# Kernel optimization log

Hardware: AMD Instinct MI355X
Metric: run time of the kernel (lower is better)

Reference implementation:

```python
import jax, jax.numpy as jnp
import numpy as np

B, L, FUT = 500, 100, 4  # dialogs, utterances per dialog, to_future_link
N = B * L
IN, HID, NC = 1024, 512, 7


def _build_graph():
    # per-dialog local edges: node i -> i (self) and i -> i+1..i+FUT (within dialog)
    i = np.arange(L)[:, None]                       # [L,1]
    off = np.arange(FUT + 1)[None, :]               # [1,FUT+1]
    tgt_local = i + off                             # [L,FUT+1]
    valid = tgt_local < L
    src_local = np.broadcast_to(i, tgt_local.shape)[valid]
    tgt_local = tgt_local[valid]                    # [E_per]
    base = (np.arange(B) * L)[:, None]              # [B,1]
    src = (base + src_local[None, :]).reshape(-1)
    tgt = (base + tgt_local[None, :]).reshape(-1)
    edges = np.stack([src, tgt], axis=0).astype(np.int64)  # [2,E], E=245000
    rng = np.random.RandomState(0)
    speakers = rng.randint(0, 2, size=N).astype(np.int64)
    rel = (speakers[src] * speakers[tgt]).astype(np.int64)  # in {0,1}
    return edges, rel


def setup_inputs() -> dict:
    key = jax.random.key(0)
    ks = jax.random.split(key, 8)
    edges, rel = _build_graph()
    s = 0.02
    return {
        "x": jax.random.normal(ks[0], (N, IN), dtype=jnp.float32),
        "edges": jnp.asarray(edges),
        "relation_type": jnp.asarray(rel),
        "w_rel": jax.random.normal(ks[1], (2, IN, HID), dtype=jnp.float32) * s,
        "w_root": jax.random.normal(ks[2], (IN, HID), dtype=jnp.float32) * s,
        "b_rgcn": jnp.zeros((HID,), jnp.float32),
        "w_gc_rel": jax.random.normal(ks[3], (HID, HID), dtype=jnp.float32) * s,
        "w_gc_root": jax.random.normal(ks[4], (HID, HID), dtype=jnp.float32) * s,
        "b_gc": jnp.zeros((HID,), jnp.float32),
        "w_skip": jax.random.normal(ks[5], (IN, HID), dtype=jnp.float32) * s,
        "b_skip": jnp.zeros((HID,), jnp.float32),
        "w_clf": jax.random.normal(ks[6], (HID, NC), dtype=jnp.float32) * s,
        "b_clf": jnp.zeros((NC,), jnp.float32),
    }


def reference(x, edges, relation_type, w_rel, w_root, b_rgcn,
              w_gc_rel, w_gc_root, b_gc, w_skip, b_skip, w_clf, b_clf):
    n = x.shape[0]
    src, tgt = edges[0], edges[1]
    # --- RGCNConv(IN, HID, 2), aggr='mean' per relation, root weight + bias ---
    x_src = x[src]  # [E, IN] gather
    h = x @ w_root + b_rgcn
    for r in range(2):
        m = (relation_type == r).astype(x.dtype)                    # [E]
        s = jax.ops.segment_sum(x_src * m[:, None], tgt, num_segments=n)  # [N,IN]
        c = jax.ops.segment_sum(m, tgt, num_segments=n)             # [N]
        mean = s / jnp.maximum(c, 1.0)[:, None]                     # scatter-mean, 0 if empty
        h = h + mean @ w_rel[r]
    # --- GraphConv(HID, HID), aggr='add': W_rel * sum_j x_j + W_root * x_i + b ---
    agg = jax.ops.segment_sum(h[src], tgt, num_segments=n)          # [N,HID]
    h2 = agg @ w_gc_rel + b_gc + h @ w_gc_root
    # --- classify(h2 + skip(x)) ---
    out = (h2 + x @ w_skip + b_skip) @ w_clf + b_clf                # [N,NC]
    return out
```

## Files before the change

kernel.cpp:

```cpp
#include <hip/hip_runtime.h>


#define DIAG_L 100
#define EPERD  490
#define NC     7
#define NROWS  50000
#define NBLK   782

using u16 = unsigned short;
using u32 = unsigned int;
typedef __bf16 bf16x8 __attribute__((ext_vector_type(8)));
typedef float  f32x4  __attribute__((ext_vector_type(4)));

__device__ __forceinline__ u16 f2b(float f) {
  u32 u = __builtin_bit_cast(u32, f);
  u32 r = (u + 0x7FFFu + ((u >> 16) & 1u)) >> 16;
  return (u16)r;
}
__device__ __forceinline__ u32 pk2(float a, float b) {
  return (u32)f2b(a) | ((u32)f2b(b) << 16);
}

__device__ __forceinline__ int pre_edges(int s) {
  int d = s - 96;
  return 5 * s - (d > 0 ? ((d * (d + 1)) >> 1) : 0);
}

__global__ __launch_bounds__(256)
void k_t1(const float* __restrict__ w_gc_root, const float* __restrict__ w_gc_rel,
          const float* __restrict__ w_clf, const float* __restrict__ b_gc,
          const float* __restrict__ b_skip, const float* __restrict__ b_clf,
          float* __restrict__ tbl, float* __restrict__ cvec) {
  int tid = blockIdx.x * 256 + threadIdx.x;
  if (tid < 8192) {
    int k = (tid >> 3) & 511, c = tid & 7, which = tid >> 12;
    float v = 0.f;
    if (c < 7) {
      const float* src = (which ? w_gc_rel : w_gc_root) + (size_t)k * 512;
      float s0 = 0.f, s1 = 0.f, s2 = 0.f, s3 = 0.f;
      for (int j = 0; j < 512; j += 4) {
        s0 += src[j]     * w_clf[(size_t)j * 7 + c];
        s1 += src[j + 1] * w_clf[(size_t)(j + 1) * 7 + c];
        s2 += src[j + 2] * w_clf[(size_t)(j + 2) * 7 + c];
        s3 += src[j + 3] * w_clf[(size_t)(j + 3) * 7 + c];
      }
      v = (s0 + s1) + (s2 + s3);
    }
    tbl[tid] = v;
  } else if (tid < 8200) {
    int c = tid - 8192;
    float v = 0.f;
    if (c < 7) {
      float s = 0.f;
      for (int j = 0; j < 512; ++j) s += (b_gc[j] + b_skip[j]) * w_clf[(size_t)j * 7 + c];
      v = s + b_clf[c];
    }
    cvec[16 + c] = v;
  }
}

__global__ __launch_bounds__(256)
void k_w64(const float* __restrict__ w_root, const float* __restrict__ w_rel,
           const float* __restrict__ w_skip, const float* __restrict__ w_clf,
           const float* __restrict__ b_rgcn, const float* __restrict__ tbl,
           u16* __restrict__ BT, float* __restrict__ cvec) {
  int tid = blockIdx.x * 256 + threadIdx.x;
  if (tid < 65536) {
    int n = tid >> 10, k = tid & 1023;
    int g = n >> 3, c = n & 7;
    float v = 0.f;
    if (c < 7 && g < 7) {
      const float* src;
      switch (g % 3) {
        case 0: src = w_root; break;
        case 1: src = w_rel; break;
        default: src = w_rel + 524288; break;
      }
      if (g == 6) src = w_skip;
      src += (size_t)k * 512;
      float s0 = 0.f, s1 = 0.f, s2 = 0.f, s3 = 0.f;
      if (g == 6) {
        for (int j = 0; j < 512; j += 4) {
          s0 += src[j]     * w_clf[(size_t)j * 7 + c];
          s1 += src[j + 1] * w_clf[(size_t)(j + 1) * 7 + c];
          s2 += src[j + 2] * w_clf[(size_t)(j + 2) * 7 + c];
          s3 += src[j + 3] * w_clf[(size_t)(j + 3) * 7 + c];
        }
      } else {
        const float* T = tbl + (g >= 3 ? 4096 : 0);
        for (int j = 0; j < 512; j += 4) {
          s0 += src[j]     * T[(j) * 8 + c];
          s1 += src[j + 1] * T[(j + 1) * 8 + c];
          s2 += src[j + 2] * T[(j + 2) * 8 + c];
          s3 += src[j + 3] * T[(j + 3) * 8 + c];
        }
      }
      v = (s0 + s1) + (s2 + s3);
    }
    BT[(size_t)n * 1024 + k] = f2b(v);
  } else if (tid < 65552) {
    int c = tid - 65536;
    const float* T = tbl + (c >= 8 ? 4096 : 0);
    int cc = c & 7;
    float s = 0.f;
    for (int k = 0; k < 512; ++k) s += b_rgcn[k] * T[k * 8 + cc];
    cvec[c] = s;
  }
}

__device__ __forceinline__ void gload16(const void* g, void* l) {
  __builtin_amdgcn_global_load_lds(
      (const __attribute__((address_space(1))) u32*)g,
      (__attribute__((address_space(3))) u32*)l, 16, 0, 0);
}

__global__ __launch_bounds__(256, 3)
void k_px2(const float* __restrict__ x, const u16* __restrict__ BT,
           float* __restrict__ P) {
  __shared__ char lds[49152];
  const int tid = threadIdx.x;
  const int w = tid >> 6, l = tid & 63;
  const int rl = l & 15, sl = l >> 4;
  const int rb = blockIdx.x << 6;
  const int sx = (rl & 7) << 4;

  const char* asrc[4]; int albase[4];
#pragma unroll
  for (int is = 0; is < 4; ++is) {
    int ci = is * 256 + tid;
    int r = ci >> 4, g = ci & 15;
    int gp = g ^ (r & 7);
    int row = rb + r; if (row > NROWS - 1) row = NROWS - 1;
    asrc[is] = (const char*)x + (size_t)row * 4096 + gp * 16;
    albase[is] = __builtin_amdgcn_readfirstlane(is * 4096 + w * 1024);
  }
  const char* bsrc[2]; int blbase[2];
#pragma unroll
  for (int is = 0; is < 2; ++is) {
    int ci = is * 256 + tid;
    int r = ci >> 3, g = ci & 7;
    int gp = g ^ (r & 7);
    bsrc[is] = (const char*)BT + (size_t)r * 2048 + gp * 16;
    blbase[is] = __builtin_amdgcn_readfirstlane(32768 + is * 4096 + w * 1024);
  }

#define STAGE(bf, kt)                                              \
  {                                                                \
    _Pragma("unroll")                                              \
    for (int is = 0; is < 4; ++is)                                 \
      gload16(asrc[is] + (kt) * 256, lds + albase[is] + (bf) * 16384); \
    _Pragma("unroll")                                              \
    for (int is = 0; is < 2; ++is)                                 \
      gload16(bsrc[is] + (kt) * 128, lds + blbase[is] + (bf) * 8192);  \
  }

  f32x4 acc[4];
#pragma unroll
  for (int nf = 0; nf < 4; ++nf) acc[nf] = f32x4{0.f, 0.f, 0.f, 0.f};

  STAGE(0, 0);
  STAGE(1, 1);
  asm volatile("s_waitcnt vmcnt(6)" ::: "memory");
  __builtin_amdgcn_s_barrier();

  for (int t = 0; t < 16; ++t) {
    const int b = t & 1;
    const char* A = lds + b * 16384 + (w * 16 + rl) * 256;
    const char* B = lds + 32768 + b * 8192 + rl * 128;
    bf16x8 af[2], bfr[2][4];
#pragma unroll
    for (int ks = 0; ks < 2; ++ks) {
      f32x4 a0 = *(const f32x4*)(A + ((ks * 128 + sl * 32) ^ sx));
      f32x4 a1 = *(const f32x4*)(A + ((ks * 128 + sl * 32 + 16) ^ sx));
      uint4 ap;
      ap.x = pk2(a0[0], a0[1]); ap.y = pk2(a0[2], a0[3]);
      ap.z = pk2(a1[0], a1[1]); ap.w = pk2(a1[2], a1[3]);
      af[ks] = __builtin_bit_cast(bf16x8, ap);
#pragma unroll
      for (int nf = 0; nf < 4; ++nf)
        bfr[ks][nf] = *(const bf16x8*)(B + nf * 2048 + ((ks * 64 + sl * 16) ^ sx));
    }
    __builtin_amdgcn_s_setprio(1);
#pragma unroll
    for (int ks = 0; ks < 2; ++ks)
#pragma unroll
      for (int nf = 0; nf < 4; ++nf)
        acc[nf] = __builtin_amdgcn_mfma_f32_16x16x32_bf16(af[ks], bfr[ks][nf],
                                                          acc[nf], 0, 0, 0);
    __builtin_amdgcn_s_setprio(0);
    __builtin_amdgcn_s_barrier();
    const int kn = (t + 2 < 16) ? t + 2 : 15;
    STAGE(b, kn);
    asm volatile("s_waitcnt vmcnt(6)" ::: "memory");
    __builtin_amdgcn_s_barrier();
  }
#undef STAGE

  const int pr = rb + w * 16 + sl * 4;
#pragma unroll
  for (int nf = 0; nf < 4; ++nf)
#pragma unroll
    for (int j = 0; j < 4; ++j)
      P[(size_t)(pr + j) * 64 + nf * 16 + rl] = acc[nf][j];
}

__global__ __launch_bounds__(128)
void k_out(const float* __restrict__ P, const int* __restrict__ rel,
           const float* __restrict__ cvec, float* __restrict__ out) {
  __shared__ float pt[64 * 100 + 16 * 100];
  float* hb = pt + 6400;
  const int d = blockIdx.x;
  const int tid = threadIdx.x;
  const float* Pd = P + (size_t)d * DIAG_L * 64;

  for (int it = tid; it < 6400; it += 128) {
    int r = it >> 6, c = it & 63;
    pt[c * 100 + r] = Pd[it];
  }
  __syncthreads();

  const int ebase = d * EPERD;
  if (tid < DIAG_L) {
    const int u = tid;
    const int slo = (u > 4) ? u - 4 : 0;
    float S0A[7], S1A[7], S0B[7], S1B[7];
#pragma unroll
    for (int c = 0; c < 7; ++c) { S0A[c] = 0.f; S1A[c] = 0.f; S0B[c] = 0.f; S1B[c] = 0.f; }
    float c0 = 0.f, c1 = 0.f;
    for (int s = slo; s <= u; ++s) {
      int r = rel[ebase + pre_edges(s) + (u - s)];
      float m0 = r ? 0.f : 1.f, m1 = 1.f - m0;
      c0 += m0; c1 += m1;
#pragma unroll
      for (int c = 0; c < 7; ++c) {
        S0A[c] += m0 * pt[(8 + c)  * 100 + s];
        S1A[c] += m1 * pt[(16 + c) * 100 + s];
        S0B[c] += m0 * pt[(32 + c) * 100 + s];
        S1B[c] += m1 * pt[(40 + c) * 100 + s];
      }
    }
    float inv0 = 1.f / fmaxf(c0, 1.f), inv1 = 1.f / fmaxf(c1, 1.f);
#pragma unroll
    for (int c = 0; c < 7; ++c) {
      hb[c * 100 + u]       = pt[c * 100 + u]        + cvec[c]     + inv0 * S0A[c] + inv1 * S1A[c];
      hb[(8 + c) * 100 + u] = pt[(24 + c) * 100 + u] + cvec[8 + c] + inv0 * S0B[c] + inv1 * S1B[c];
    }
  }
  __syncthreads();

  if (tid < DIAG_L) {
    const int t = tid;
    const int slo = (t > 4) ? t - 4 : 0;
    float o[7];
#pragma unroll
    for (int c = 0; c < 7; ++c)
      o[c] = hb[c * 100 + t] + pt[(48 + c) * 100 + t] + cvec[16 + c];
    for (int s = slo; s <= t; ++s) {
#pragma unroll
      for (int c = 0; c < 7; ++c) o[c] += hb[(8 + c) * 100 + s];
    }
    float* op = out + ((size_t)d * DIAG_L + t) * NC;
#pragma unroll
    for (int c = 0; c < 7; ++c) op[c] = o[c];
  }
}

extern "C" void kernel_launch(void* const* d_in, const int* in_sizes, int n_in,
                              void* d_out, int out_size, void* d_ws, size_t ws_size,
                              hipStream_t stream) {
  const float* x         = (const float*)d_in[0];
  const int*   rel       = (const int*)d_in[2];
  const float* w_rel     = (const float*)d_in[3];
  const float* w_root    = (const float*)d_in[4];
  const float* b_rgcn    = (const float*)d_in[5];
  const float* w_gc_rel  = (const float*)d_in[6];
  const float* w_gc_root = (const float*)d_in[7];
  const float* b_gc      = (const float*)d_in[8];
  const float* w_skip    = (const float*)d_in[9];
  const float* b_skip    = (const float*)d_in[10];
  const float* w_clf     = (const float*)d_in[11];
  const float* b_clf     = (const float*)d_in[12];
  float* out = (float*)d_out;

  char* ws = (char*)d_ws;
  float* P    = (float*)(ws);
  u16*   BT   = (u16*)(ws + 12845056);
  float* tbl  = (float*)(ws + 12976128);
  float* cvec = (float*)(ws + 13008896);

  k_t1<<<33, 256, 0, stream>>>(w_gc_root, w_gc_rel, w_clf, b_gc, b_skip, b_clf, tbl, cvec);
  k_w64<<<257, 256, 0, stream>>>(w_root, w_rel, w_skip, w_clf, b_rgcn, tbl, BT, cvec);
  k_px2<<<NBLK, 256, 0, stream>>>(x, BT, P);
  k_out<<<500, 128, 0, stream>>>(P, rel, cvec, out);
}
```

Measured before the change: 89.65 us.

## Register-stage A tile as bf16 in LDS and parallelize weight-folding kernels

The main GEMM kernel now loads x through registers, converts it to bf16 before writing to LDS, and halves the LDS footprint so more blocks fit per CU (launch bounds raised to 5). This removes the per-iteration fp32 LDS reads and conversion inside the MFMA loop. The two weight-folding precompute kernels are restructured to spread each dot product across lanes with shuffle reductions, raising their parallelism. The trade-off is that A loads are now synchronous register loads rather than async global-to-LDS copies, and more VGPRs are held across the compute.

```diff
diff --git a/kernel.cpp b/kernel.cpp
--- a/kernel.cpp
+++ b/kernel.cpp
@@ -26,50 +26,57 @@
   return 5 * s - (d > 0 ? ((d * (d + 1)) >> 1) : 0);
 }
 
+__global__ __launch_bounds__(64)
+void k_t1n(const float* __restrict__ w_gc_root, const float* __restrict__ w_gc_rel,
+           const float* __restrict__ w_clf, const float* __restrict__ b_gc,
+           const float* __restrict__ b_skip, const float* __restrict__ b_clf,
+           float* __restrict__ tbl, float* __restrict__ cvec) {
+  const int bid = blockIdx.x, l = threadIdx.x;
+  if (bid < 1024) {
+    const int which = bid & 1, k = bid >> 1;
+    const float* src = (which ? w_gc_rel : w_gc_root) + (size_t)k * 512;
+    float p[7] = {0.f, 0.f, 0.f, 0.f, 0.f, 0.f, 0.f};
+#pragma unroll
+    for (int jj = 0; jj < 8; ++jj) {
+      int j = jj * 64 + l;
+      float sv = src[j];
+      const float* wc = w_clf + (size_t)j * 7;
+#pragma unroll
+      for (int c = 0; c < 7; ++c) p[c] += sv * wc[c];
+    }
+#pragma unroll
+    for (int c = 0; c < 7; ++c)
+      for (int d = 32; d; d >>= 1) p[c] += __shfl_xor(p[c], d);
+    if (l == 0) {
+      float* tr = tbl + which * 4096 + k * 8;
+#pragma unroll
+      for (int c = 0; c < 7; ++c) tr[c] = p[c];
+      tr[7] = 0.f;
+    }
+  } else {
+    const int c = bid - 1024;
+    float s = 0.f;
+#pragma unroll
+    for (int jj = 0; jj < 8; ++jj) {
+      int j = jj * 64 + l;
+      s += (b_gc[j] + b_skip[j]) * w_clf[(size_t)j * 7 + c];
+    }
+    for (int d = 32; d; d >>= 1) s += __shfl_xor(s, d);
+    if (l == 0) cvec[16 + c] = s + b_clf[c];
+  }
+}
+
 __global__ __launch_bounds__(256)
-void k_t1(const float* __restrict__ w_gc_root, const float* __restrict__ w_gc_rel,
-          const float* __restrict__ w_clf, const float* __restrict__ b_gc,
-          const float* __restrict__ b_skip, const float* __restrict__ b_clf,
-          float* __restrict__ tbl, float* __restrict__ cvec) {
-  int tid = blockIdx.x * 256 + threadIdx.x;
-  if (tid < 8192) {
-    int k = (tid >> 3) & 511, c = tid & 7, which = tid >> 12;
-    float v = 0.f;
-    if (c < 7) {
-      const float* src = (which ? w_gc_rel : w_gc_root) + (size_t)k * 512;
-      float s0 = 0.f, s1 = 0.f, s2 = 0.f, s3 = 0.f;
-      for (int j = 0; j < 512; j += 4) {
-        s0 += src[j]     * w_clf[(size_t)j * 7 + c];
-        s1 += src[j + 1] * w_clf[(size_t)(j + 1) * 7 + c];
-        s2 += src[j + 2] * w_clf[(size_t)(j + 2) * 7 + c];
-        s3 += src[j + 3] * w_clf[(size_t)(j + 3) * 7 + c];
-      }
-      v = (s0 + s1) + (s2 + s3);
-    }
-    tbl[tid] = v;
-  } else if (tid < 8200) {
-    int c = tid - 8192;
-    float v = 0.f;
-    if (c < 7) {
-      float s = 0.f;
-      for (int j = 0; j < 512; ++j) s += (b_gc[j] + b_skip[j]) * w_clf[(size_t)j * 7 + c];
-      v = s + b_clf[c];
-    }
-    cvec[16 + c] = v;
-  }
-}
-
-__global__ __launch_bounds__(256)
-void k_w64(const float* __restrict__ w_root, const float* __restrict__ w_rel,
-           const float* __restrict__ w_skip, const float* __restrict__ w_clf,
-           const float* __restrict__ b_rgcn, const float* __restrict__ tbl,
-           u16* __restrict__ BT, float* __restrict__ cvec) {
-  int tid = blockIdx.x * 256 + threadIdx.x;
-  if (tid < 65536) {
-    int n = tid >> 10, k = tid & 1023;
-    int g = n >> 3, c = n & 7;
-    float v = 0.f;
-    if (c < 7 && g < 7) {
+void k_w64n(const float* __restrict__ w_root, const float* __restrict__ w_rel,
+            const float* __restrict__ w_skip, const float* __restrict__ w_clf,
+            const float* __restrict__ b_rgcn, const float* __restrict__ tbl,
+            u16* __restrict__ BT, float* __restrict__ cvec) {
+  const int bid = blockIdx.x;
+  if (bid < 1024) {
+    const int k = bid, tid = threadIdx.x;
+    const int n = tid >> 2, jq = tid & 3, g = n >> 3, c = n & 7;
+    float p = 0.f;
+    if (g < 7 && c < 7) {
       const float* src;
       switch (g % 3) {
         case 0: src = w_root; break;
@@ -78,33 +85,38 @@
       }
       if (g == 6) src = w_skip;
       src += (size_t)k * 512;
-      float s0 = 0.f, s1 = 0.f, s2 = 0.f, s3 = 0.f;
       if (g == 6) {
-        for (int j = 0; j < 512; j += 4) {
-          s0 += src[j]     * w_clf[(size_t)j * 7 + c];
-          s1 += src[j + 1] * w_clf[(size_t)(j + 1) * 7 + c];
-          s2 += src[j + 2] * w_clf[(size_t)(j + 2) * 7 + c];
-          s3 += src[j + 3] * w_clf[(size_t)(j + 3) * 7 + c];
+#pragma unroll 4
+        for (int i = 0; i < 128; ++i) {
+          int j = jq * 128 + i;
+          p += src[j] * w_clf[(size_t)j * 7 + c];
         }
       } else {
         const float* T = tbl + (g >= 3 ? 4096 : 0);
-        for (int j = 0; j < 512; j += 4) {
-          s0 += src[j]     * T[(j) * 8 + c];
-          s1 += src[j + 1] * T[(j + 1) * 8 + c];
-          s2 += src[j + 2] * T[(j + 2) * 8 + c];
-          s3 += src[j + 3] * T[(j + 3) * 8 + c];
+#pragma unroll 4
+        for (int i = 0; i < 128; ++i) {
+          int j = jq * 128 + i;
+          p += src[j] * T[j * 8 + c];
         }
       }
-      v = (s0 + s1) + (s2 + s3);
-    }
-    BT[(size_t)n * 1024 + k] = f2b(v);
-  } else if (tid < 65552) {
-    int c = tid - 65536;
-    const float* T = tbl + (c >= 8 ? 4096 : 0);
-    int cc = c & 7;
-    float s = 0.f;
-    for (int k = 0; k < 512; ++k) s += b_rgcn[k] * T[k * 8 + cc];
-    cvec[c] = s;
+    }
+    p += __shfl_xor(p, 1); p += __shfl_xor(p, 2);
+    if (jq == 0) BT[(size_t)n * 1024 + k] = f2b(p);
+  } else {
+    const int idx = bid - 1024;
+    const int l = threadIdx.x;
+    if (l < 64) {
+      const float* T = tbl + (idx >= 8 ? 4096 : 0);
+      const int cc = idx & 7;
+      float s = 0.f;
+#pragma unroll
+      for (int jj = 0; jj < 8; ++jj) {
+        int j = jj * 64 + l;
+        s += b_rgcn[j] * T[j * 8 + cc];
+      }
+      for (int d = 32; d; d >>= 1) s += __shfl_xor(s, d);
+      if (l == 0) cvec[idx] = s;
+    }
   }
 }
 
@@ -114,87 +126,85 @@
       (__attribute__((address_space(3))) u32*)l, 16, 0, 0);
 }
 
-__global__ __launch_bounds__(256, 3)
-void k_px2(const float* __restrict__ x, const u16* __restrict__ BT,
+__global__ __launch_bounds__(256, 5)
+void k_px3(const float* __restrict__ x, const u16* __restrict__ BT,
            float* __restrict__ P) {
-  __shared__ char lds[49152];
+  __shared__ char lds[32768];
   const int tid = threadIdx.x;
   const int w = tid >> 6, l = tid & 63;
   const int rl = l & 15, sl = l >> 4;
   const int rb = blockIdx.x << 6;
   const int sx = (rl & 7) << 4;
 
-  const char* asrc[4]; int albase[4];
-#pragma unroll
-  for (int is = 0; is < 4; ++is) {
-    int ci = is * 256 + tid;
-    int r = ci >> 4, g = ci & 15;
-    int gp = g ^ (r & 7);
-    int row = rb + r; if (row > NROWS - 1) row = NROWS - 1;
-    asrc[is] = (const char*)x + (size_t)row * 4096 + gp * 16;
-    albase[is] = __builtin_amdgcn_readfirstlane(is * 4096 + w * 1024);
-  }
+  const int ar = tid >> 2, ac4 = tid & 3;
+  int arow = rb + ar; if (arow > NROWS - 1) arow = NROWS - 1;
+  const char* axp = (const char*)x + (size_t)arow * 4096 + ac4 * 64;
+  const int aw0 = ar * 128 + ((ac4 * 32) ^ ((ar & 7) << 4));
+  const int aw1 = ar * 128 + ((ac4 * 32 + 16) ^ ((ar & 7) << 4));
+
   const char* bsrc[2]; int blbase[2];
 #pragma unroll
   for (int is = 0; is < 2; ++is) {
     int ci = is * 256 + tid;
-    int r = ci >> 3, g = ci & 7;
-    int gp = g ^ (r & 7);
+    int r = ci >> 3, g = ci & 7, gp = g ^ (r & 7);
     bsrc[is] = (const char*)BT + (size_t)r * 2048 + gp * 16;
-    blbase[is] = __builtin_amdgcn_readfirstlane(32768 + is * 4096 + w * 1024);
-  }
-
-#define STAGE(bf, kt)                                              \
-  {                                                                \
-    _Pragma("unroll")                                              \
-    for (int is = 0; is < 4; ++is)                                 \
-      gload16(asrc[is] + (kt) * 256, lds + albase[is] + (bf) * 16384); \
-    _Pragma("unroll")                                              \
-    for (int is = 0; is < 2; ++is)                                 \
-      gload16(bsrc[is] + (kt) * 128, lds + blbase[is] + (bf) * 8192);  \
-  }
+    blbase[is] = __builtin_amdgcn_readfirstlane(16384 + is * 4096 + w * 1024);
+  }
+
+  float4 av[4];
+#define ALOAD(kt) { av[0] = *(const float4*)(axp + (kt) * 256);      \
+                    av[1] = *(const float4*)(axp + (kt) * 256 + 16); \
+                    av[2] = *(const float4*)(axp + (kt) * 256 + 32); \
+                    av[3] = *(const float4*)(axp + (kt) * 256 + 48); }
+#define AWRITE(bf) { uint4 q0, q1;                                   \
+    q0.x = pk2(av[0].x, av[0].y); q0.y = pk2(av[0].z, av[0].w);      \
+    q0.z = pk2(av[1].x, av[1].y); q0.w = pk2(av[1].z, av[1].w);      \
+    q1.x = pk2(av[2].x, av[2].y); q1.y = pk2(av[2].z, av[2].w);      \
+    q1.z = pk2(av[3].x, av[3].y); q1.w = pk2(av[3].z, av[3].w);      \
+    *(uint4*)(lds + (bf) * 8192 + aw0) = q0;                         \
+    *(uint4*)(lds + (bf) * 8192 + aw1) = q1; }
+#define BSTAGE(bf, kt) {                                             \
+    gload16(bsrc[0] + (kt) * 128, lds + blbase[0] + (bf) * 8192);    \
+    gload16(bsrc[1] + (kt) * 128, lds + blbase[1] + (bf) * 8192); }
 
   f32x4 acc[4];
 #pragma unroll
   for (int nf = 0; nf < 4; ++nf) acc[nf] = f32x4{0.f, 0.f, 0.f, 0.f};
 
-  STAGE(0, 0);
-  STAGE(1, 1);
-  asm volatile("s_waitcnt vmcnt(6)" ::: "memory");
+  ALOAD(0); BSTAGE(0, 0); AWRITE(0);
+  ALOAD(1); BSTAGE(1, 1); AWRITE(1);
+  asm volatile("s_waitcnt lgkmcnt(0)" ::: "memory");
   __builtin_amdgcn_s_barrier();
 
   for (int t = 0; t < 16; ++t) {
     const int b = t & 1;
-    const char* A = lds + b * 16384 + (w * 16 + rl) * 256;
-    const char* B = lds + 32768 + b * 8192 + rl * 128;
-    bf16x8 af[2], bfr[2][4];
+    const char* Ab = lds + b * 8192 + (w * 16 + rl) * 128;
+    const char* Bb = lds + 16384 + b * 8192 + rl * 128;
+    const int kn = (t + 2 < 16) ? t + 2 : 15;
+    ALOAD(kn);
 #pragma unroll
     for (int ks = 0; ks < 2; ++ks) {
-      f32x4 a0 = *(const f32x4*)(A + ((ks * 128 + sl * 32) ^ sx));
-      f32x4 a1 = *(const f32x4*)(A + ((ks * 128 + sl * 32 + 16) ^ sx));
-      uint4 ap;
-      ap.x = pk2(a0[0], a0[1]); ap.y = pk2(a0[2], a0[3]);
-      ap.z = pk2(a1[0], a1[1]); ap.w = pk2(a1[2], a1[3]);
-      af[ks] = __builtin_bit_cast(bf16x8, ap);
-#pragma unroll
-      for (int nf = 0; nf < 4; ++nf)
-        bfr[ks][nf] = *(const bf16x8*)(B + nf * 2048 + ((ks * 64 + sl * 16) ^ sx));
-    }
-    __builtin_amdgcn_s_setprio(1);
-#pragma unroll
-    for (int ks = 0; ks < 2; ++ks)
-#pragma unroll
-      for (int nf = 0; nf < 4; ++nf)
-        acc[nf] = __builtin_amdgcn_mfma_f32_16x16x32_bf16(af[ks], bfr[ks][nf],
-                                                          acc[nf], 0, 0, 0);
-    __builtin_amdgcn_s_setprio(0);
+      const int ko = (ks * 64 + sl * 16) ^ sx;
+      bf16x8 af = *(const bf16x8*)(Ab + ko);
+      bf16x8 b0 = *(const bf16x8*)(Bb + ko);
+      bf16x8 b1 = *(const bf16x8*)(Bb + 2048 + ko);
+      bf16x8 b2 = *(const bf16x8*)(Bb + 4096 + ko);
+      bf16x8 b3 = *(const bf16x8*)(Bb + 6144 + ko);
+      acc[0] = __builtin_amdgcn_mfma_f32_16x16x32_bf16(af, b0, acc[0], 0, 0, 0);
+      acc[1] = __builtin_amdgcn_mfma_f32_16x16x32_bf16(af, b1, acc[1], 0, 0, 0);
+      acc[2] = __builtin_amdgcn_mfma_f32_16x16x32_bf16(af, b2, acc[2], 0, 0, 0);
+      acc[3] = __builtin_amdgcn_mfma_f32_16x16x32_bf16(af, b3, acc[3], 0, 0, 0);
+    }
     __builtin_amdgcn_s_barrier();
-    const int kn = (t + 2 < 16) ? t + 2 : 15;
-    STAGE(b, kn);
-    asm volatile("s_waitcnt vmcnt(6)" ::: "memory");
+    BSTAGE(b, kn);
+    AWRITE(b);
+    asm volatile("s_waitcnt lgkmcnt(0)" ::: "memory");
     __builtin_amdgcn_s_barrier();
   }
-#undef STAGE
+  asm volatile("s_waitcnt vmcnt(0)" ::: "memory");
+#undef ALOAD
+#undef AWRITE
+#undef BSTAGE
 
   const int pr = rb + w * 16 + sl * 4;
 #pragma unroll
@@ -288,8 +298,8 @@
   float* tbl  = (float*)(ws + 12976128);
   float* cvec = (float*)(ws + 13008896);
 
-  k_t1<<<33, 256, 0, stream>>>(w_gc_root, w_gc_rel, w_clf, b_gc, b_skip, b_clf, tbl, cvec);
-  k_w64<<<257, 256, 0, stream>>>(w_root, w_rel, w_skip, w_clf, b_rgcn, tbl, BT, cvec);
-  k_px2<<<NBLK, 256, 0, stream>>>(x, BT, P);
+  k_t1n<<<1031, 64, 0, stream>>>(w_gc_root, w_gc_rel, w_clf, b_gc, b_skip, b_clf, tbl, cvec);
+  k_w64n<<<1040, 256, 0, stream>>>(w_root, w_rel, w_skip, w_clf, b_rgcn, tbl, BT, cvec);
+  k_px3<<<NBLK, 256, 0, stream>>>(x, BT, P);
   k_out<<<500, 128, 0, stream>>>(P, rel, cvec, out);
 }
```

Result: faster. 82.12 us, median of 2 (-8.4%).
